# Optimization experiments

Hardware: AMD Instinct MI355X
Metric: run time of the kernel (lower is better)

The kernel has to match this reference:

```python
import jax, jax.numpy as jnp
import numpy as np

B, N, D, E = 32, 4096, 128, 24576


def setup_inputs() -> dict:
    key = jax.random.key(0)
    k1, k2, k3 = jax.random.split(key, 3)
    x = jax.random.normal(k1, (B, N, D), dtype=jnp.float32)
    edge_index = jax.random.randint(k2, (2, E), 0, N, dtype=jnp.int32)
    # gate_linear: Linear(2*D, 1)
    W = jax.random.normal(k3, (1, 2 * D), dtype=jnp.float32) * 0.05
    b = jnp.zeros((1,), dtype=jnp.float32)
    return {"x": x, "edge_index": edge_index, "W": W, "b": b}


def reference(x, edge_index, W, b):
    # x: [B, N, D]; edge_index: [2, E]
    src, dst = edge_index[0], edge_index[1]
    x_src = x[:, src]              # [B, E, D]
    x_dst = x[:, dst]              # [B, E, D]
    d = x.shape[-1]
    # Linear on concat([x_src, x_dst]) == x_src @ Ws^T + x_dst @ Wd^T + b
    Ws, Wd = W[:, :d], W[:, d:]
    scores = (jnp.einsum('bed,od->beo', x_src, Ws)
              + jnp.einsum('bed,od->beo', x_dst, Wd) + b)  # [B, E, 1]
    attention = jax.nn.sigmoid(scores)
    msg = x_src * attention        # [B, E, D]
    out = jnp.zeros_like(x).at[:, dst].add(msg)  # scatter_add over node axis
    return out
```

## Files before the change

kernel.cpp:

```cpp
#include <hip/hip_runtime.h>
#include <hip/hip_bf16.h>


#define NN 4096
#define BB 32
#define DD 128
#define SLOT 32

typedef float f4v __attribute__((ext_vector_type(4)));

__global__ __launch_bounds__(1024) void zero_deg_k(int* __restrict__ deg) {
    deg[blockIdx.x * 1024 + threadIdx.x] = 0;
}

__global__ __launch_bounds__(256) void dots_fill_k(
        const float* __restrict__ x, const float* __restrict__ W,
        const int* __restrict__ src, const int* __restrict__ dst, int E,
        int* __restrict__ deg, int* __restrict__ slots,
        float* __restrict__ dsrc, float* __restrict__ ddst) {
    const int nDotBlocks = BB * NN / 64;
    if (blockIdx.x < nDotBlocks) {
        const int wave = threadIdx.x >> 6;
        const int lane = threadIdx.x & 63;
        const int half = lane >> 5;
        const int l32  = lane & 31;
        const int row0 = blockIdx.x * 64 + wave * 16;
        const float4 ws = *reinterpret_cast<const float4*>(W + l32 * 4);
        const float4 wd = *reinterpret_cast<const float4*>(W + DD + l32 * 4);
#pragma unroll
        for (int i = 0; i < 8; ++i) {
            const int row = row0 + 2 * i + half;
            const float4 v = *reinterpret_cast<const float4*>(x + (size_t)row * DD + l32 * 4);
            float ps = v.x * ws.x + v.y * ws.y + v.z * ws.z + v.w * ws.w;
            float pd = v.x * wd.x + v.y * wd.y + v.z * wd.z + v.w * wd.w;
            for (int off = 16; off; off >>= 1) {
                ps += __shfl_xor(ps, off, 64);
                pd += __shfl_xor(pd, off, 64);
            }
            if (l32 == 0) {
                dsrc[row] = ps;
                ddst[row] = pd;
            }
        }
    } else {
        const int e = (blockIdx.x - nDotBlocks) * 256 + threadIdx.x;
        if (e < E) {
            const int d = dst[e];
            const int pos = atomicAdd(&deg[d], 1);
            if (pos < SLOT) slots[d * SLOT + pos] = src[e];
        }
    }
}

__global__ __launch_bounds__(256) void gather_k(const float* __restrict__ x,
                                                const int* __restrict__ deg,
                                                const int* __restrict__ slots,
                                                const float* __restrict__ dsrc,
                                                const float* __restrict__ ddst,
                                                const float* __restrict__ bptr,
                                                float* __restrict__ out) {
    const int sl   = blockIdx.x;
    const int xcd  = sl & 7;
    const int idx  = sl >> 3;
    const int b    = ((idx >> 8) << 3) | xcd;
    const int nblk = idx & 255;
    const int wave = threadIdx.x >> 6;
    const int lane = threadIdx.x & 63;
    const int half = lane >> 5;
    const int l32  = lane & 31;
    const int n0   = nblk * 16 + wave * 4;
    const int nA   = n0 + half;
    const int nB   = n0 + 2 + half;

    const float bias = bptr[0];
    const float* xb  = x + (size_t)b * NN * DD;
    const float* dsb = dsrc + (size_t)b * NN;

    const int4 dv4 = *reinterpret_cast<const int4*>(deg + n0);
    const int cnt0 = dv4.x < SLOT ? dv4.x : SLOT;
    const int cnt1 = dv4.y < SLOT ? dv4.y : SLOT;
    const int cnt2 = dv4.z < SLOT ? dv4.z : SLOT;
    const int cnt3 = dv4.w < SLOT ? dv4.w : SLOT;
    const int cA   = half ? cnt1 : cnt0;
    const int cB   = half ? cnt3 : cnt2;

    const float4 dd4 = *reinterpret_cast<const float4*>(ddst + ((size_t)b << 12) + n0);
    const float sdA = half ? dd4.y : dd4.x;
    const float sdB = half ? dd4.w : dd4.z;

    int   sAl = 0, sBl = 0;
    float aAl = 0.f, aBl = 0.f;
    if (l32 < cA) sAl = slots[nA * SLOT + l32];
    if (l32 < cB) sBl = slots[nB * SLOT + l32];
    if (l32 < cA) {
        const float sc = dsb[sAl] + sdA + bias;
        aAl = 1.0f / (1.0f + __expf(-sc));
    }
    if (l32 < cB) {
        const float sc = dsb[sBl] + sdB + bias;
        aBl = 1.0f / (1.0f + __expf(-sc));
    }

    float4 acc0 = make_float4(0.f, 0.f, 0.f, 0.f);
    float4 acc1 = make_float4(0.f, 0.f, 0.f, 0.f);
    float4 acc2 = make_float4(0.f, 0.f, 0.f, 0.f);
    float4 acc3 = make_float4(0.f, 0.f, 0.f, 0.f);
    const int cmA  = cnt0 > cnt1 ? cnt0 : cnt1;
    const int cmB  = cnt2 > cnt3 ? cnt2 : cnt3;
    const int cmax = cmA > cmB ? cmA : cmB;
    for (int j = 0; j < cmax; j += 2) {
        const int   s0 = __shfl(sAl, j + half, 64);
        const float a0 = __shfl(aAl, j + half, 64);
        const int   s1 = __shfl(sAl, 32 + j + half, 64);
        const float a1 = __shfl(aAl, 32 + j + half, 64);
        const int   s2 = __shfl(sBl, j + half, 64);
        const float a2 = __shfl(aBl, j + half, 64);
        const int   s3 = __shfl(sBl, 32 + j + half, 64);
        const float a3 = __shfl(aBl, 32 + j + half, 64);
        const float4 v0 = *reinterpret_cast<const float4*>(xb + (size_t)s0 * DD + l32 * 4);
        const float4 v1 = *reinterpret_cast<const float4*>(xb + (size_t)s1 * DD + l32 * 4);
        const float4 v2 = *reinterpret_cast<const float4*>(xb + (size_t)s2 * DD + l32 * 4);
        const float4 v3 = *reinterpret_cast<const float4*>(xb + (size_t)s3 * DD + l32 * 4);
        acc0.x += a0 * v0.x; acc0.y += a0 * v0.y; acc0.z += a0 * v0.z; acc0.w += a0 * v0.w;
        acc1.x += a1 * v1.x; acc1.y += a1 * v1.y; acc1.z += a1 * v1.z; acc1.w += a1 * v1.w;
        acc2.x += a2 * v2.x; acc2.y += a2 * v2.y; acc2.z += a2 * v2.z; acc2.w += a2 * v2.w;
        acc3.x += a3 * v3.x; acc3.y += a3 * v3.y; acc3.z += a3 * v3.z; acc3.w += a3 * v3.w;
    }
    acc0.x += __shfl_xor(acc0.x, 32, 64);
    acc0.y += __shfl_xor(acc0.y, 32, 64);
    acc0.z += __shfl_xor(acc0.z, 32, 64);
    acc0.w += __shfl_xor(acc0.w, 32, 64);
    acc1.x += __shfl_xor(acc1.x, 32, 64);
    acc1.y += __shfl_xor(acc1.y, 32, 64);
    acc1.z += __shfl_xor(acc1.z, 32, 64);
    acc1.w += __shfl_xor(acc1.w, 32, 64);
    acc2.x += __shfl_xor(acc2.x, 32, 64);
    acc2.y += __shfl_xor(acc2.y, 32, 64);
    acc2.z += __shfl_xor(acc2.z, 32, 64);
    acc2.w += __shfl_xor(acc2.w, 32, 64);
    acc3.x += __shfl_xor(acc3.x, 32, 64);
    acc3.y += __shfl_xor(acc3.y, 32, 64);
    acc3.z += __shfl_xor(acc3.z, 32, 64);
    acc3.w += __shfl_xor(acc3.w, 32, 64);
    f4v rA, rB;
    rA.x = half ? acc1.x : acc0.x;
    rA.y = half ? acc1.y : acc0.y;
    rA.z = half ? acc1.z : acc0.z;
    rA.w = half ? acc1.w : acc0.w;
    rB.x = half ? acc3.x : acc2.x;
    rB.y = half ? acc3.y : acc2.y;
    rB.z = half ? acc3.z : acc2.z;
    rB.w = half ? acc3.w : acc2.w;
    f4v* pA = reinterpret_cast<f4v*>(out + ((size_t)((b << 12) | nA)) * DD + l32 * 4);
    f4v* pB = reinterpret_cast<f4v*>(out + ((size_t)((b << 12) | nB)) * DD + l32 * 4);
    __builtin_nontemporal_store(rA, pA);
    __builtin_nontemporal_store(rB, pB);
}

extern "C" void kernel_launch(void* const* d_in, const int* in_sizes, int n_in,
                              void* d_out, int out_size, void* d_ws, size_t ws_size,
                              hipStream_t stream) {
    const float* x    = (const float*)d_in[0];
    const int*   ei   = (const int*)d_in[1];
    const float* W    = (const float*)d_in[2];
    const float* bias = (const float*)d_in[3];
    float* out = (float*)d_out;

    const int E = in_sizes[1] / 2;
    const int* src = ei;
    const int* dst = ei + E;

    int* deg     = (int*)d_ws;
    int* slots   = deg + NN;
    float* dsrc  = (float*)(slots + NN * SLOT);
    float* ddst  = dsrc + BB * NN;

    zero_deg_k<<<NN / 1024, 1024, 0, stream>>>(deg);
    dots_fill_k<<<BB * NN / 64 + (E + 255) / 256, 256, 0, stream>>>(
        x, W, src, dst, E, deg, slots, dsrc, ddst);
    gather_k<<<BB * NN / 16, 256, 0, stream>>>(x, deg, slots, dsrc, ddst, bias, out);
}
```

Before: 139.5 us.

## Gather neighbor features from a bf16 copy of x and split uneven-degree loops

The dot-product pass now also writes a bf16 copy of x to workspace, and the gather kernel reads neighbor rows from this copy, halving the bytes fetched per gathered row. The gather loop is split into a shared part up to the smaller max-degree and separate tails for each node pair, which avoids loads for padding slots. The degree zeroing kernel is replaced with hipMemsetAsync. In exchange, an extra 64MB write is added and accumulated values lose precision from bf16 rounding, which may break tolerance.

```diff
diff --git a/kernel.cpp b/kernel.cpp
--- a/kernel.cpp
+++ b/kernel.cpp
@@ -1,5 +1,4 @@
 #include <hip/hip_runtime.h>
-#include <hip/hip_bf16.h>
 
 
 #define NN 4096
@@ -8,16 +7,23 @@
 #define SLOT 32
 
 typedef float f4v __attribute__((ext_vector_type(4)));
-
-__global__ __launch_bounds__(1024) void zero_deg_k(int* __restrict__ deg) {
-    deg[blockIdx.x * 1024 + threadIdx.x] = 0;
+typedef unsigned short u16x4 __attribute__((ext_vector_type(4)));
+
+__device__ __forceinline__ unsigned short f2bf(float f) {
+    unsigned u = __float_as_uint(f);
+    u += 0x7FFF + ((u >> 16) & 1);
+    return (unsigned short)(u >> 16);
+}
+__device__ __forceinline__ float bf2f(unsigned short h) {
+    return __uint_as_float(((unsigned)h) << 16);
 }
 
 __global__ __launch_bounds__(256) void dots_fill_k(
         const float* __restrict__ x, const float* __restrict__ W,
         const int* __restrict__ src, const int* __restrict__ dst, int E,
         int* __restrict__ deg, int* __restrict__ slots,
-        float* __restrict__ dsrc, float* __restrict__ ddst) {
+        float* __restrict__ dsrc, float* __restrict__ ddst,
+        unsigned short* __restrict__ xb16) {
     const int nDotBlocks = BB * NN / 64;
     if (blockIdx.x < nDotBlocks) {
         const int wave = threadIdx.x >> 6;
@@ -31,6 +37,9 @@
         for (int i = 0; i < 8; ++i) {
             const int row = row0 + 2 * i + half;
             const float4 v = *reinterpret_cast<const float4*>(x + (size_t)row * DD + l32 * 4);
+            u16x4 hv;
+            hv.x = f2bf(v.x); hv.y = f2bf(v.y); hv.z = f2bf(v.z); hv.w = f2bf(v.w);
+            *reinterpret_cast<u16x4*>(xb16 + (size_t)row * DD + l32 * 4) = hv;
             float ps = v.x * ws.x + v.y * ws.y + v.z * ws.z + v.w * ws.w;
             float pd = v.x * wd.x + v.y * wd.y + v.z * wd.z + v.w * wd.w;
             for (int off = 16; off; off >>= 1) {
@@ -52,7 +61,7 @@
     }
 }
 
-__global__ __launch_bounds__(256) void gather_k(const float* __restrict__ x,
+__global__ __launch_bounds__(256) void gather_k(const unsigned short* __restrict__ xb16,
                                                 const int* __restrict__ deg,
                                                 const int* __restrict__ slots,
                                                 const float* __restrict__ dsrc,
@@ -73,7 +82,7 @@
     const int nB   = n0 + 2 + half;
 
     const float bias = bptr[0];
-    const float* xb  = x + (size_t)b * NN * DD;
+    const unsigned short* xb = xb16 + (size_t)b * NN * DD;
     const float* dsb = dsrc + (size_t)b * NN;
 
     const int4 dv4 = *reinterpret_cast<const int4*>(deg + n0);
@@ -107,8 +116,10 @@
     float4 acc3 = make_float4(0.f, 0.f, 0.f, 0.f);
     const int cmA  = cnt0 > cnt1 ? cnt0 : cnt1;
     const int cmB  = cnt2 > cnt3 ? cnt2 : cnt3;
-    const int cmax = cmA > cmB ? cmA : cmB;
-    for (int j = 0; j < cmax; j += 2) {
+    const int cmin = cmA < cmB ? cmA : cmB;
+
+    int j = 0;
+    for (; j < cmin; j += 2) {
         const int   s0 = __shfl(sAl, j + half, 64);
         const float a0 = __shfl(aAl, j + half, 64);
         const int   s1 = __shfl(sAl, 32 + j + half, 64);
@@ -117,15 +128,36 @@
         const float a2 = __shfl(aBl, j + half, 64);
         const int   s3 = __shfl(sBl, 32 + j + half, 64);
         const float a3 = __shfl(aBl, 32 + j + half, 64);
-        const float4 v0 = *reinterpret_cast<const float4*>(xb + (size_t)s0 * DD + l32 * 4);
-        const float4 v1 = *reinterpret_cast<const float4*>(xb + (size_t)s1 * DD + l32 * 4);
-        const float4 v2 = *reinterpret_cast<const float4*>(xb + (size_t)s2 * DD + l32 * 4);
-        const float4 v3 = *reinterpret_cast<const float4*>(xb + (size_t)s3 * DD + l32 * 4);
-        acc0.x += a0 * v0.x; acc0.y += a0 * v0.y; acc0.z += a0 * v0.z; acc0.w += a0 * v0.w;
-        acc1.x += a1 * v1.x; acc1.y += a1 * v1.y; acc1.z += a1 * v1.z; acc1.w += a1 * v1.w;
-        acc2.x += a2 * v2.x; acc2.y += a2 * v2.y; acc2.z += a2 * v2.z; acc2.w += a2 * v2.w;
-        acc3.x += a3 * v3.x; acc3.y += a3 * v3.y; acc3.z += a3 * v3.z; acc3.w += a3 * v3.w;
-    }
+        const u16x4 v0 = *reinterpret_cast<const u16x4*>(xb + (size_t)s0 * DD + l32 * 4);
+        const u16x4 v1 = *reinterpret_cast<const u16x4*>(xb + (size_t)s1 * DD + l32 * 4);
+        const u16x4 v2 = *reinterpret_cast<const u16x4*>(xb + (size_t)s2 * DD + l32 * 4);
+        const u16x4 v3 = *reinterpret_cast<const u16x4*>(xb + (size_t)s3 * DD + l32 * 4);
+        acc0.x += a0 * bf2f(v0.x); acc0.y += a0 * bf2f(v0.y); acc0.z += a0 * bf2f(v0.z); acc0.w += a0 * bf2f(v0.w);
+        acc1.x += a1 * bf2f(v1.x); acc1.y += a1 * bf2f(v1.y); acc1.z += a1 * bf2f(v1.z); acc1.w += a1 * bf2f(v1.w);
+        acc2.x += a2 * bf2f(v2.x); acc2.y += a2 * bf2f(v2.y); acc2.z += a2 * bf2f(v2.z); acc2.w += a2 * bf2f(v2.w);
+        acc3.x += a3 * bf2f(v3.x); acc3.y += a3 * bf2f(v3.y); acc3.z += a3 * bf2f(v3.z); acc3.w += a3 * bf2f(v3.w);
+    }
+    for (int jA = j; jA < cmA; jA += 2) {
+        const int   s0 = __shfl(sAl, jA + half, 64);
+        const float a0 = __shfl(aAl, jA + half, 64);
+        const int   s1 = __shfl(sAl, 32 + jA + half, 64);
+        const float a1 = __shfl(aAl, 32 + jA + half, 64);
+        const u16x4 v0 = *reinterpret_cast<const u16x4*>(xb + (size_t)s0 * DD + l32 * 4);
+        const u16x4 v1 = *reinterpret_cast<const u16x4*>(xb + (size_t)s1 * DD + l32 * 4);
+        acc0.x += a0 * bf2f(v0.x); acc0.y += a0 * bf2f(v0.y); acc0.z += a0 * bf2f(v0.z); acc0.w += a0 * bf2f(v0.w);
+        acc1.x += a1 * bf2f(v1.x); acc1.y += a1 * bf2f(v1.y); acc1.z += a1 * bf2f(v1.z); acc1.w += a1 * bf2f(v1.w);
+    }
+    for (int jB = j; jB < cmB; jB += 2) {
+        const int   s2 = __shfl(sBl, jB + half, 64);
+        const float a2 = __shfl(aBl, jB + half, 64);
+        const int   s3 = __shfl(sBl, 32 + jB + half, 64);
+        const float a3 = __shfl(aBl, 32 + jB + half, 64);
+        const u16x4 v2 = *reinterpret_cast<const u16x4*>(xb + (size_t)s2 * DD + l32 * 4);
+        const u16x4 v3 = *reinterpret_cast<const u16x4*>(xb + (size_t)s3 * DD + l32 * 4);
+        acc2.x += a2 * bf2f(v2.x); acc2.y += a2 * bf2f(v2.y); acc2.z += a2 * bf2f(v2.z); acc2.w += a2 * bf2f(v2.w);
+        acc3.x += a3 * bf2f(v3.x); acc3.y += a3 * bf2f(v3.y); acc3.z += a3 * bf2f(v3.z); acc3.w += a3 * bf2f(v3.w);
+    }
+
     acc0.x += __shfl_xor(acc0.x, 32, 64);
     acc0.y += __shfl_xor(acc0.y, 32, 64);
     acc0.z += __shfl_xor(acc0.z, 32, 64);
@@ -142,6 +174,7 @@
     acc3.y += __shfl_xor(acc3.y, 32, 64);
     acc3.z += __shfl_xor(acc3.z, 32, 64);
     acc3.w += __shfl_xor(acc3.w, 32, 64);
+
     f4v rA, rB;
     rA.x = half ? acc1.x : acc0.x;
     rA.y = half ? acc1.y : acc0.y;
@@ -174,9 +207,10 @@
     int* slots   = deg + NN;
     float* dsrc  = (float*)(slots + NN * SLOT);
     float* ddst  = dsrc + BB * NN;
-
-    zero_deg_k<<<NN / 1024, 1024, 0, stream>>>(deg);
+    unsigned short* xb16 = (unsigned short*)(ddst + BB * NN);
+
+    hipMemsetAsync(deg, 0, NN * sizeof(int), stream);
     dots_fill_k<<<BB * NN / 64 + (E + 255) / 256, 256, 0, stream>>>(
-        x, W, src, dst, E, deg, slots, dsrc, ddst);
-    gather_k<<<BB * NN / 16, 256, 0, stream>>>(x, deg, slots, dsrc, ddst, bias, out);
-}
+        x, W, src, dst, E, deg, slots, dsrc, ddst, xb16);
+    gather_k<<<BB * NN / 16, 256, 0, stream>>>(xb16, deg, slots, dsrc, ddst, bias, out);
+}
```

New measurement: 143.8 us. 3.0% more time.
